# Kernel tuning notes

Measured on AMD Instinct MI355X. Metric: run time of the kernel, lower is better.

The kernel has to match this reference:

```python
import jax, jax.numpy as jnp
import numpy as np

LEAK = 0.01  # torch LeakyReLU default negative_slope

def lrelu(x):
    return jnp.where(x >= 0, x, LEAK * x)

def edge_conv(x, src, dst, ea, W1, b1, W2, b2):
    # message: cat(x_i=target, x_j=source, edge_attr) -> Linear -> LeakyReLU -> Linear
    m = jnp.concatenate([x[dst], x[src], ea], axis=1)          # [E, 2F+Fe]
    h = lrelu(m @ W1 + b1) @ W2 + b2                            # [E, H]
    n = x.shape[0]
    agg = jnp.full((n, h.shape[1]), jnp.inf, h.dtype).at[dst].min(h)  # scatter-min at target
    return jnp.where(jnp.isfinite(agg), agg, jnp.zeros_like(agg))     # empty nodes -> 0


def setup_inputs() -> dict:
    key = jax.random.key(0)
    ks = jax.random.split(key, 20)
    B, N, E = 4, 20000, 640000
    NF, AD, EF, H = 2, 1, 1, 8
    inp = {
        "node_features": jax.random.randint(ks[0], (B, N, NF), 0, 10, dtype=jnp.int32),
        "actions": jax.random.normal(ks[1], (B, N), dtype=jnp.float32),
        "edge_index": jax.random.randint(ks[2], (B, 2, E), 0, N, dtype=jnp.int64),
        "edge_features": jax.random.normal(ks[3], (B, E, EF), dtype=jnp.float32),
    }
    d0 = NF + AD  # 3
    def lin(k, fin, fout):
        s = 1.0 / np.sqrt(fin)
        k1, k2 = jax.random.split(k)
        return (jax.random.uniform(k1, (fin, fout), jnp.float32, -s, s),
                jax.random.uniform(k2, (fout,), jnp.float32, -s, s))
    inp["c1_W1"], inp["c1_b1"] = lin(ks[4], 2 * d0 + EF, H)
    inp["c1_W2"], inp["c1_b2"] = lin(ks[5], H, H)
    inp["c2_W1"], inp["c2_b1"] = lin(ks[6], 2 * H + 1, H)
    inp["c2_W2"], inp["c2_b2"] = lin(ks[7], H, H)
    inp["c3_W1"], inp["c3_b1"] = lin(ks[8], 2 * H + 1, H)
    inp["c3_W2"], inp["c3_b2"] = lin(ks[9], H, H)
    inp["lin_W"], inp["lin_b"] = lin(ks[10], d0 + H, 1)
    return inp


def reference(node_features, actions, edge_index, edge_features,
              c1_W1, c1_b1, c1_W2, c1_b2,
              c2_W1, c2_b1, c2_W2, c2_b2,
              c3_W1, c3_b1, c3_W2, c3_b2,
              lin_W, lin_b):
    # x = int(node_features) concat actions  -> float
    x0 = jnp.concatenate([node_features.astype(jnp.int32).astype(jnp.float32),
                          actions[..., None]], axis=-1)  # [B,N,3]

    def per_graph(x0g, eig, eag):
        src, dst = eig[0], eig[1]  # flow source_to_target: x_j=src, x_i=dst
        h = lrelu(edge_conv(x0g, src, dst, eag, c1_W1, c1_b1, c1_W2, c1_b2))
        h = lrelu(edge_conv(h, src, dst, eag, c2_W1, c2_b1, c2_W2, c2_b2))
        h = lrelu(edge_conv(h, src, dst, eag, c3_W1, c3_b1, c3_W2, c3_b2))
        xc = jnp.concatenate([x0g, h], axis=1)  # [N, 3+8]
        return jnp.sum(xc, axis=0)              # sum-pool over nodes

    pooled = jax.vmap(per_graph)(x0, edge_index, edge_features)  # [B, 11]
    return pooled @ lin_W + lin_b  # [B, 1]
```

## Files before the change

### kernel.cpp

```cpp
#include <hip/hip_runtime.h>
#include <hip/hip_cooperative_groups.h>

#define LEAK 0.01f
#define BS 128
#define PCHUNK 4096
#define PT 512
#define CT 512
#define MAXNB 256
#define CPGMAX 256
#define BARSTRIDE 64

__device__ __forceinline__ float lrelu(float v) {
    return v >= 0.f ? v : LEAK * v;
}

__device__ __forceinline__ unsigned int fmin_encode(float x) {
    unsigned int u = __float_as_uint(x);
    return (u & 0x80000000u) ? ~u : (u | 0x80000000u);
}
__device__ __forceinline__ float fmin_decode(unsigned int k) {
    unsigned int u = (k & 0x80000000u) ? (k ^ 0x80000000u) : ~k;
    return __uint_as_float(u);
}

__device__ __forceinline__ unsigned int bf16_rne(float f) {
    unsigned int u = __float_as_uint(f);
    return (u + 0x7FFFu + ((u >> 16) & 1u)) >> 16;
}

__device__ __forceinline__ void block_add(float c, float* dst) {
    __shared__ float wsum[8];
#pragma unroll
    for (int off = 32; off > 0; off >>= 1) c += __shfl_down(c, off, 64);
    int lane = threadIdx.x & 63;
    int wave = threadIdx.x >> 6;
    if (lane == 0) wsum[wave] = c;
    __syncthreads();
    if (threadIdx.x == 0) {
        float s = 0.f;
        int nw = blockDim.x >> 6;
        for (int w = 0; w < nw; ++w) s += wsum[w];
        atomicAdd(dst, s);
    }
}

__device__ __forceinline__ void graph_barrier(int* bar, int target) {
    __syncthreads();
    if (threadIdx.x == 0) {
        __threadfence();
        __hip_atomic_fetch_add(bar, 1, __ATOMIC_RELEASE, __HIP_MEMORY_SCOPE_AGENT);
        while (__hip_atomic_load(bar, __ATOMIC_RELAXED, __HIP_MEMORY_SCOPE_AGENT) <
               target)
            __builtin_amdgcn_s_sleep(2);
        __threadfence();
    }
    __syncthreads();
}


__device__ __forceinline__ void init_body(
    const int* __restrict__ nf, const float* __restrict__ act,
    const float* __restrict__ W1, const float* __restrict__ b1,
    const float* __restrict__ lw, const float* __restrict__ lb,
    float* __restrict__ a1, unsigned short* __restrict__ a2,
    float* __restrict__ out, int N, int b, int ib) {
    int t = threadIdx.x;
    int n = ib * PT + t;
    float c = 0.f;
    if (n < N) {
        size_t i = (size_t)b * N + n;
        float x0 = (float)nf[i * 2 + 0];
        float x1 = (float)nf[i * 2 + 1];
        float x2 = act[i];
        float v1[8], v2[8];
#pragma unroll
        for (int j = 0; j < 8; ++j) {
            v1[j] = b1[j] + x0 * W1[0 * 8 + j] + x1 * W1[1 * 8 + j] + x2 * W1[2 * 8 + j];
            v2[j] =         x0 * W1[3 * 8 + j] + x1 * W1[4 * 8 + j] + x2 * W1[5 * 8 + j];
        }
        float4* o1 = (float4*)(a1 + i * 8);
        o1[0] = make_float4(v1[0], v1[1], v1[2], v1[3]);
        o1[1] = make_float4(v1[4], v1[5], v1[6], v1[7]);
        unsigned int w[4];
#pragma unroll
        for (int q = 0; q < 4; ++q)
            w[q] = bf16_rne(v2[2 * q]) | (bf16_rne(v2[2 * q + 1]) << 16);
        *(int4*)(a2 + i * 8) = make_int4(w[0], w[1], w[2], w[3]);
        c = x0 * lw[0] + x1 * lw[1] + x2 * lw[2];
        if (n == 0) c += lb[0];
    }
    block_add(c, &out[b]);
}

__device__ __forceinline__ void part_body(
    const int* __restrict__ ei, const float* __restrict__ ea,
    int2* __restrict__ pairs, int* __restrict__ ofs,
    int E, int NB, int CPG, int b, int c,
    int* __restrict__ lc, int* __restrict__ lofs, int* __restrict__ ts) {
    int t = threadIdx.x;
    for (int i = t; i < NB; i += PT) lc[i] = 0;
    __syncthreads();

    int e0 = c * PCHUNK;
    int end = min(e0 + PCHUNK, E);
    const int* srow = ei + (size_t)b * 2 * E;
    const int* drow = srow + E;

    int pk[PCHUNK / PT];
#pragma unroll
    for (int j = 0; j < PCHUNK / PT; ++j) {
        int e = e0 + j * PT + t;
        int p = -1;
        if (e < end) {
            int d = drow[e];
            int bin = d >> 7;
            int r = atomicAdd(&lc[bin], 1);
            p = bin | ((d & 127) << 10) | (r << 17);
        }
        pk[j] = p;
    }
    __syncthreads();

    int v = (t < NB) ? lc[t] : 0;
    ts[t] = v;
    __syncthreads();
    int incl = v;
    for (int off = 1; off < PT; off <<= 1) {
        int add = (t >= off) ? ts[t - off] : 0;
        __syncthreads();
        incl += add;
        ts[t] = incl;
        __syncthreads();
    }
    if (t < NB) lofs[t] = incl - v;
    if (t == PT - 1) lofs[NB] = incl;
    __syncthreads();

    for (int i = t; i <= NB; i += PT) {
        int w = lofs[i];
        ofs[((size_t)b * (NB + 1) + i) * CPG + c] = w;
        if (i < NB) lc[i] = w;
    }
    __syncthreads();

    size_t pbase = (size_t)b * E + e0;
#pragma unroll
    for (int j = 0; j < PCHUNK / PT; ++j) {
        int e = e0 + j * PT + t;
        if (e < end) {
            int p = pk[j];
            int bin = p & 1023;
            int dl = (p >> 10) & 127;
            int r = p >> 17;
            int pos = lc[bin] + r;
            pairs[pbase + pos] =
                make_int2(srow[e] | (dl << 16), __float_as_int(ea[(size_t)b * E + e]));
        }
    }
}

__device__ __forceinline__ void conv_edge_compute(
    const float* we, const float* bb, const float* __restrict__ W2,
    int2 p, int4 raw, const float* __restrict__ a1s,
    unsigned int* __restrict__ acc) {
    int dl = (p.x >> 16) & 127;
    float eav = __int_as_float(p.y);
    unsigned int wq[4] = {(unsigned int)raw.x, (unsigned int)raw.y,
                          (unsigned int)raw.z, (unsigned int)raw.w};
    float a2v[8];
#pragma unroll
    for (int q = 0; q < 4; ++q) {
        a2v[2 * q]     = __uint_as_float(wq[q] << 16);
        a2v[2 * q + 1] = __uint_as_float(wq[q] & 0xFFFF0000u);
    }
    float h1[8];
#pragma unroll
    for (int j = 0; j < 8; ++j) {
        h1[j] = a1s[dl * 9 + j] + a2v[j];
        h1[j] = fmaf(eav, we[j], h1[j]);
        h1[j] = lrelu(h1[j]);
    }
    float h2[8];
#pragma unroll
    for (int j = 0; j < 8; ++j) h2[j] = bb[j];
#pragma unroll
    for (int kk = 0; kk < 8; ++kk) {
        float hk = h1[kk];
#pragma unroll
        for (int j = 0; j < 8; ++j) h2[j] = fmaf(hk, W2[kk * 8 + j], h2[j]);
    }
#pragma unroll
    for (int j = 0; j < 8; ++j)
        atomicMin(&acc[dl * 9 + j], fmin_encode(h2[j]));
}

__device__ __forceinline__ void conv_edges_runs(
    const unsigned short* __restrict__ a2g, const float* we, const float* bb,
    const float* __restrict__ W2, const int2* __restrict__ pairsg,
    const int* __restrict__ ofb, int CPG,
    const float* __restrict__ a1s, unsigned int* __restrict__ acc,
    int* __restrict__ rs, int* __restrict__ re) {
    int t = threadIdx.x;
    for (int c = t; c < CPG; c += CT) {
        rs[c] = ofb[c];
        re[c] = ofb[CPG + c];
    }
    __syncthreads();
    int sw = t >> 5, sub = t & 31;
    const int nsw = CT >> 5;
    for (int c = sw; c < CPG; c += nsw) {
        int cb = c * PCHUNK;
        int k1 = cb + re[c];
        for (int k = cb + rs[c] + sub; k < k1; k += 32) {
            int2 p = pairsg[k];
            int4 v = *(const int4*)(a2g + (size_t)(p.x & 0xFFFF) * 8);
            conv_edge_compute(we, bb, W2, p, v, a1s, acc);
        }
    }
}

__device__ __forceinline__ void conv_mid_body(
    const float* __restrict__ a1, const unsigned short* __restrict__ a2,
    const float* __restrict__ w1e, const float* __restrict__ W2,
    const float* __restrict__ b2,
    const float* __restrict__ nW1, const float* __restrict__ nb1,
    const int* __restrict__ ofs, const int2* __restrict__ pairs,
    float* __restrict__ na1, unsigned short* __restrict__ na2,
    int N, int NB, int CPG, int E, int b, int bin,
    float* __restrict__ a1s, unsigned int* __restrict__ acc,
    int* __restrict__ rs, int* __restrict__ re) {
    int n0 = bin << 7;
    int nCnt = min(BS, N - n0);
    int t = threadIdx.x;
    size_t node0 = (size_t)b * N + n0;

    for (int i = t; i < nCnt * 8; i += CT)
        a1s[(i >> 3) * 9 + (i & 7)] = a1[node0 * 8 + i];
    for (int i = t; i < BS * 9; i += CT) acc[i] = 0xFFFFFFFFu;
    float we[8], bb[8];
#pragma unroll
    for (int j = 0; j < 8; ++j) { we[j] = w1e[j]; bb[j] = b2[j]; }
    __syncthreads();

    conv_edges_runs(a2 + (size_t)b * N * 8, we, bb, W2,
                    pairs + (size_t)b * E,
                    ofs + ((size_t)b * (NB + 1) + bin) * CPG,
                    CPG, a1s, acc, rs, re);
    __syncthreads();

    for (int i = t; i < nCnt * 8; i += CT) {
        float v = fmin_decode(acc[(i >> 3) * 9 + (i & 7)]);
        unsigned int u = __float_as_uint(v);
        if ((u & 0x7F800000u) == 0x7F800000u) v = 0.f;
        a1s[(i >> 3) * 9 + (i & 7)] = lrelu(v);
    }
    __syncthreads();

    for (int nh = t; nh < nCnt * 2; nh += CT) {
        int node = nh >> 1, half = nh & 1;
        float h[8];
#pragma unroll
        for (int j = 0; j < 8; ++j) h[j] = a1s[node * 9 + j];
        float v[8];
#pragma unroll
        for (int j = 0; j < 8; ++j) v[j] = half ? 0.f : nb1[j];
        const float* Wbase = nW1 + (half ? 64 : 0);
#pragma unroll
        for (int k = 0; k < 8; ++k) {
            float hk = h[k];
#pragma unroll
            for (int j = 0; j < 8; ++j) v[j] = fmaf(hk, Wbase[k * 8 + j], v[j]);
        }
        if (half) {
            unsigned int w[4];
#pragma unroll
            for (int q = 0; q < 4; ++q)
                w[q] = bf16_rne(v[2 * q]) | (bf16_rne(v[2 * q + 1]) << 16);
            *(int4*)(na2 + (node0 + node) * 8) = make_int4(w[0], w[1], w[2], w[3]);
        } else {
            float4* o = (float4*)(na1 + (node0 + node) * 8);
            o[0] = make_float4(v[0], v[1], v[2], v[3]);
            o[1] = make_float4(v[4], v[5], v[6], v[7]);
        }
    }
    __syncthreads();
}

__device__ __forceinline__ void conv_final_body(
    const float* __restrict__ a1, const unsigned short* __restrict__ a2,
    const float* __restrict__ w1e, const float* __restrict__ W2,
    const float* __restrict__ b2, const float* __restrict__ lw,
    const int* __restrict__ ofs, const int2* __restrict__ pairs,
    float* __restrict__ out, int N, int NB, int CPG, int E, int b, int bin,
    float* __restrict__ a1s, unsigned int* __restrict__ acc,
    int* __restrict__ rs, int* __restrict__ re) {
    int n0 = bin << 7;
    int nCnt = min(BS, N - n0);
    int t = threadIdx.x;
    size_t node0 = (size_t)b * N + n0;

    for (int i = t; i < nCnt * 8; i += CT)
        a1s[(i >> 3) * 9 + (i & 7)] = a1[node0 * 8 + i];
    for (int i = t; i < BS * 9; i += CT) acc[i] = 0xFFFFFFFFu;
    float we[8], bb[8];
#pragma unroll
    for (int j = 0; j < 8; ++j) { we[j] = w1e[j]; bb[j] = b2[j]; }
    __syncthreads();

    conv_edges_runs(a2 + (size_t)b * N * 8, we, bb, W2,
                    pairs + (size_t)b * E,
                    ofs + ((size_t)b * (NB + 1) + bin) * CPG,
                    CPG, a1s, acc, rs, re);
    __syncthreads();

    float c = 0.f;
    if (t < nCnt) {
#pragma unroll
        for (int j = 0; j < 8; ++j) {
            float v = fmin_decode(acc[t * 9 + j]);
            unsigned int u = __float_as_uint(v);
            if ((u & 0x7F800000u) == 0x7F800000u) v = 0.f;
            c = fmaf(lrelu(v), lw[3 + j], c);
        }
    }
    __syncthreads();
    block_add(c, &out[b]);
}


struct MegaParams {
    const int* ei; const float* ea;
    int2* pairs; int* ofs;
    const int* nf; const float* act;
    const float* W11; const float* b11; const float* W21; const float* b21;
    const float* W12; const float* b12; const float* W22; const float* b22;
    const float* W13; const float* b13; const float* W23; const float* b23;
    const float* lw; const float* lb;
    float* a1A; unsigned short* a2A; float* a1B; unsigned short* a2B;
    float* out;
    int* bar;
    int E, N, NB, CPG, initBlocks;
};

__global__ __launch_bounds__(512, 8) void mega_kernel(MegaParams P) {
    __shared__ int lc[MAXNB];
    __shared__ int lofs[MAXNB + 1];
    __shared__ int ts[PT];
    __shared__ float a1s[BS * 9];
    __shared__ unsigned int acc[BS * 9];
    __shared__ int rs[CPGMAX];
    __shared__ int re[CPGMAX];
    int b = blockIdx.y, bx = blockIdx.x;
    int* bar = P.bar + b * BARSTRIDE;
    const int gx = gridDim.x;

    if (bx < P.CPG)
        part_body(P.ei, P.ea, P.pairs, P.ofs, P.E, P.NB, P.CPG, b, bx, lc, lofs, ts);
    else if (bx - P.CPG < P.initBlocks)
        init_body(P.nf, P.act, P.W11, P.b11, P.lw, P.lb, P.a1A, P.a2A, P.out,
                  P.N, b, bx - P.CPG);
    graph_barrier(bar, gx);
    if (bx < P.NB)
        conv_mid_body(P.a1A, P.a2A, P.W11 + 6 * 8, P.W21, P.b21, P.W12, P.b12,
                      P.ofs, P.pairs, P.a1B, P.a2B, P.N, P.NB, P.CPG, P.E,
                      b, bx, a1s, acc, rs, re);
    graph_barrier(bar, gx * 2);
    if (bx < P.NB)
        conv_mid_body(P.a1B, P.a2B, P.W12 + 16 * 8, P.W22, P.b22, P.W13, P.b13,
                      P.ofs, P.pairs, P.a1A, P.a2A, P.N, P.NB, P.CPG, P.E,
                      b, bx, a1s, acc, rs, re);
    graph_barrier(bar, gx * 3);
    if (bx < P.NB)
        conv_final_body(P.a1A, P.a2A, P.W13 + 16 * 8, P.W23, P.b23, P.lw,
                        P.ofs, P.pairs, P.out, P.N, P.NB, P.CPG, P.E,
                        b, bx, a1s, acc, rs, re);
}


__global__ __launch_bounds__(PT) void part_init_kernel(
    const int* __restrict__ ei, const float* __restrict__ ea,
    int2* __restrict__ pairs, int* __restrict__ ofs,
    const int* __restrict__ nf, const float* __restrict__ act,
    const float* __restrict__ W1, const float* __restrict__ b1,
    const float* __restrict__ lw, const float* __restrict__ lb,
    float* __restrict__ a1, unsigned short* __restrict__ a2,
    float* __restrict__ out, int E, int N, int NB, int CPG) {
    __shared__ int lc[MAXNB];
    __shared__ int lofs[MAXNB + 1];
    __shared__ int ts[PT];
    int b = blockIdx.y;
    if (blockIdx.x >= CPG) {
        init_body(nf, act, W1, b1, lw, lb, a1, a2, out, N, b, blockIdx.x - CPG);
        return;
    }
    part_body(ei, ea, pairs, ofs, E, NB, CPG, b, blockIdx.x, lc, lofs, ts);
}

__global__ __launch_bounds__(CT) void conv_mid_kernel(
    const float* __restrict__ a1, const unsigned short* __restrict__ a2,
    const float* __restrict__ w1e, const float* __restrict__ W2,
    const float* __restrict__ b2,
    const float* __restrict__ nW1, const float* __restrict__ nb1,
    const int* __restrict__ ofs, const int2* __restrict__ pairs,
    float* __restrict__ na1, unsigned short* __restrict__ na2,
    int N, int NB, int CPG, int E) {
    __shared__ float a1s[BS * 9];
    __shared__ unsigned int acc[BS * 9];
    __shared__ int rs[CPGMAX];
    __shared__ int re[CPGMAX];
    conv_mid_body(a1, a2, w1e, W2, b2, nW1, nb1, ofs, pairs, na1, na2,
                  N, NB, CPG, E, blockIdx.y, blockIdx.x, a1s, acc, rs, re);
}

__global__ __launch_bounds__(CT) void conv_final_kernel(
    const float* __restrict__ a1, const unsigned short* __restrict__ a2,
    const float* __restrict__ w1e, const float* __restrict__ W2,
    const float* __restrict__ b2, const float* __restrict__ lw,
    const int* __restrict__ ofs, const int2* __restrict__ pairs,
    float* __restrict__ out, int N, int NB, int CPG, int E) {
    __shared__ float a1s[BS * 9];
    __shared__ unsigned int acc[BS * 9];
    __shared__ int rs[CPGMAX];
    __shared__ int re[CPGMAX];
    conv_final_body(a1, a2, w1e, W2, b2, lw, ofs, pairs, out,
                    N, NB, CPG, E, blockIdx.y, blockIdx.x, a1s, acc, rs, re);
}


__global__ __launch_bounds__(256) void node_init_kernel(
    const int* __restrict__ nf, const float* __restrict__ act,
    float* __restrict__ x0, int BN) {
    int tid = blockIdx.x * blockDim.x + threadIdx.x;
    if (tid >= BN) return;
    x0[tid * 3 + 0] = (float)nf[tid * 2 + 0];
    x0[tid * 3 + 1] = (float)nf[tid * 2 + 1];
    x0[tid * 3 + 2] = act[tid];
}

template <int D>
__global__ __launch_bounds__(256) void edge_conv_kernel(
    const float* __restrict__ x, const int* __restrict__ ei,
    const float* __restrict__ ea,
    const float* __restrict__ W1, const float* __restrict__ b1,
    const float* __restrict__ W2, const float* __restrict__ b2,
    unsigned int* __restrict__ agg, int E, int N, int B) {
    int tid = blockIdx.x * blockDim.x + threadIdx.x;
    if (tid >= B * E) return;
    int b = tid / E;
    int e = tid - b * E;
    const int* eb = ei + (size_t)b * 2 * E;
    int s = eb[e];
    int d = eb[E + e];
    const float* xi = x + ((size_t)b * N + d) * D;
    const float* xj = x + ((size_t)b * N + s) * D;
    constexpr int M = 2 * D + 1;
    float m[M];
#pragma unroll
    for (int k = 0; k < D; ++k) { m[k] = xi[k]; m[D + k] = xj[k]; }
    m[2 * D] = ea[(size_t)b * E + e];
    float h1[8];
#pragma unroll
    for (int j = 0; j < 8; ++j) h1[j] = b1[j];
#pragma unroll
    for (int k = 0; k < M; ++k) {
        float mk = m[k];
#pragma unroll
        for (int j = 0; j < 8; ++j) h1[j] = fmaf(mk, W1[k * 8 + j], h1[j]);
    }
#pragma unroll
    for (int j = 0; j < 8; ++j) h1[j] = lrelu(h1[j]);
    float h2[8];
#pragma unroll
    for (int j = 0; j < 8; ++j) h2[j] = b2[j];
#pragma unroll
    for (int k = 0; k < 8; ++k) {
        float hk = h1[k];
#pragma unroll
        for (int j = 0; j < 8; ++j) h2[j] = fmaf(hk, W2[k * 8 + j], h2[j]);
    }
    unsigned int* ag = agg + ((size_t)b * N + d) * 8;
#pragma unroll
    for (int j = 0; j < 8; ++j) atomicMin(&ag[j], fmin_encode(h2[j]));
}

__global__ __launch_bounds__(256) void finalize_kernel(
    unsigned int* __restrict__ agg, int total) {
    int tid = blockIdx.x * blockDim.x + threadIdx.x;
    if (tid >= total) return;
    float v = fmin_decode(agg[tid]);
    unsigned int u = __float_as_uint(v);
    if ((u & 0x7F800000u) == 0x7F800000u) v = 0.f;
    ((float*)agg)[tid] = lrelu(v);
}

__global__ __launch_bounds__(256) void pool_kernel(
    const float* __restrict__ x0, const float* __restrict__ h,
    const float* __restrict__ lw, const float* __restrict__ lb,
    float* __restrict__ out, int N) {
    int b = blockIdx.y;
    int n = blockIdx.x * blockDim.x + threadIdx.x;
    float c = 0.f;
    if (n < N) {
        const float* x = x0 + ((size_t)b * N + n) * 3;
        const float* hh = h + ((size_t)b * N + n) * 8;
        c = x[0] * lw[0] + x[1] * lw[1] + x[2] * lw[2];
#pragma unroll
        for (int k = 0; k < 8; ++k) c = fmaf(hh[k], lw[3 + k], c);
        if (n == 0) c += lb[0];
    }
    block_add(c, &out[b]);
}


static inline size_t align256(size_t x) { return (x + 255) & ~(size_t)255; }

extern "C" void kernel_launch(void* const* d_in, const int* in_sizes, int n_in,
                              void* d_out, int out_size, void* d_ws, size_t ws_size,
                              hipStream_t stream) {
    const int B = 4;
    const int N = in_sizes[1] / B;
    const int E = in_sizes[2] / (2 * B);

    const int*   nf  = (const int*)d_in[0];
    const float* act = (const float*)d_in[1];
    const int*   ei  = (const int*)d_in[2];
    const float* ea  = (const float*)d_in[3];
    const float* c1_W1 = (const float*)d_in[4];
    const float* c1_b1 = (const float*)d_in[5];
    const float* c1_W2 = (const float*)d_in[6];
    const float* c1_b2 = (const float*)d_in[7];
    const float* c2_W1 = (const float*)d_in[8];
    const float* c2_b1 = (const float*)d_in[9];
    const float* c2_W2 = (const float*)d_in[10];
    const float* c2_b2 = (const float*)d_in[11];
    const float* c3_W1 = (const float*)d_in[12];
    const float* c3_b1 = (const float*)d_in[13];
    const float* c3_W2 = (const float*)d_in[14];
    const float* c3_b2 = (const float*)d_in[15];
    const float* lw    = (const float*)d_in[16];
    const float* lb    = (const float*)d_in[17];
    float* out = (float*)d_out;

    const int BN = B * N;
    const int BE = B * E;
    const int NB = (N + BS - 1) / BS;
    const int CPG = (E + PCHUNK - 1) / PCHUNK;
    const int initBlocks = (N + PT - 1) / PT;

    char* ws = (char*)d_ws;
    size_t off = 0;
    float* a1A = (float*)(ws + off);           off += align256((size_t)BN * 8 * 4);
    float* a1B = (float*)(ws + off);           off += align256((size_t)BN * 8 * 4);
    unsigned short* a2A = (unsigned short*)(ws + off); off += align256((size_t)BN * 8 * 2);
    unsigned short* a2B = (unsigned short*)(ws + off); off += align256((size_t)BN * 8 * 2);
    int* ofs    = (int*)(ws + off);    off += align256((size_t)B * (NB + 1) * CPG * 4);
    int2* pairs = (int2*)(ws + off);   off += align256((size_t)BE * 8);
    float* x0   = (float*)(ws + off);  off += align256((size_t)BN * 3 * 4);
    int* bar    = (int*)(ws + off);    off += align256((size_t)B * BARSTRIDE * 4);
    const bool useFast = (off <= ws_size) && (NB <= MAXNB) && (CPG <= CPGMAX) &&
                         (N <= 32768);

    hipMemsetAsync(out, 0, (size_t)B * sizeof(float), stream);

    if (useFast) {
        const int gx = (CPG + initBlocks > NB) ? (CPG + initBlocks) : NB;

        int dev = 0;
        hipGetDevice(&dev);
        int numCU = 0;
        hipDeviceGetAttribute(&numCU, hipDeviceAttributeMultiprocessorCount, dev);
        int occ = 0;
        hipOccupancyMaxActiveBlocksPerMultiprocessor(&occ, mega_kernel, 512, 0);
        const bool canCoop = (occ > 0) && ((size_t)occ * (size_t)numCU >=
                                           (size_t)gx * (size_t)B);

        if (canCoop) {
            hipMemsetAsync(bar, 0, (size_t)B * BARSTRIDE * sizeof(int), stream);
            MegaParams P;
            P.ei = ei; P.ea = ea; P.pairs = pairs; P.ofs = ofs;
            P.nf = nf; P.act = act;
            P.W11 = c1_W1; P.b11 = c1_b1; P.W21 = c1_W2; P.b21 = c1_b2;
            P.W12 = c2_W1; P.b12 = c2_b1; P.W22 = c2_W2; P.b22 = c2_b2;
            P.W13 = c3_W1; P.b13 = c3_b1; P.W23 = c3_W2; P.b23 = c3_b2;
            P.lw = lw; P.lb = lb;
            P.a1A = a1A; P.a2A = a2A; P.a1B = a1B; P.a2B = a2B;
            P.out = out; P.bar = bar;
            P.E = E; P.N = N; P.NB = NB; P.CPG = CPG; P.initBlocks = initBlocks;
            void* args[] = {&P};
            hipLaunchCooperativeKernel((void*)mega_kernel, dim3(gx, B),
                                       dim3(512), args, 0, stream);
        } else {
            dim3 pgrid(CPG + initBlocks, B);
            dim3 cgrid(NB, B);
            part_init_kernel<<<pgrid, PT, 0, stream>>>(
                ei, ea, pairs, ofs, nf, act, c1_W1, c1_b1, lw, lb,
                a1A, a2A, out, E, N, NB, CPG);
            conv_mid_kernel<<<cgrid, CT, 0, stream>>>(
                a1A, a2A, c1_W1 + 6 * 8, c1_W2, c1_b2, c2_W1, c2_b1,
                ofs, pairs, a1B, a2B, N, NB, CPG, E);
            conv_mid_kernel<<<cgrid, CT, 0, stream>>>(
                a1B, a2B, c2_W1 + 16 * 8, c2_W2, c2_b2, c3_W1, c3_b1,
                ofs, pairs, a1A, a2A, N, NB, CPG, E);
            conv_final_kernel<<<cgrid, CT, 0, stream>>>(
                a1A, a2A, c3_W1 + 16 * 8, c3_W2, c3_b2, lw,
                ofs, pairs, out, N, NB, CPG, E);
        }
    } else {
        const int egrid = (BE + 255) / 256;
        const int aggTotal = BN * 8;
        const int agrid = (aggTotal + 255) / 256;
        const size_t aggBytes = (size_t)aggTotal * 4;
        unsigned int* uA = (unsigned int*)a1A;
        unsigned int* uB = (unsigned int*)a1B;

        node_init_kernel<<<(BN + 255) / 256, 256, 0, stream>>>(nf, act, x0, BN);

        hipMemsetAsync(uA, 0xFF, aggBytes, stream);
        edge_conv_kernel<3><<<egrid, 256, 0, stream>>>(
            x0, ei, ea, c1_W1, c1_b1, c1_W2, c1_b2, uA, E, N, B);
        finalize_kernel<<<agrid, 256, 0, stream>>>(uA, aggTotal);

        hipMemsetAsync(uB, 0xFF, aggBytes, stream);
        edge_conv_kernel<8><<<egrid, 256, 0, stream>>>(
            (const float*)uA, ei, ea, c2_W1, c2_b1, c2_W2, c2_b2, uB, E, N, B);
        finalize_kernel<<<agrid, 256, 0, stream>>>(uB, aggTotal);

        hipMemsetAsync(uA, 0xFF, aggBytes, stream);
        edge_conv_kernel<8><<<egrid, 256, 0, stream>>>(
            (const float*)uB, ei, ea, c3_W1, c3_b1, c3_W2, c3_b2, uA, E, N, B);
        finalize_kernel<<<agrid, 256, 0, stream>>>(uA, aggTotal);

        dim3 plgrid((N + 255) / 256, B);
        pool_kernel<<<plgrid, 256, 0, stream>>>(x0, (const float*)uA, lw, lb, out, N);
    }
}
```

Baseline: 208.6 us.

## Compact partitioned edge pairs into contiguous per-bin ranges before conv layers

Adds a compaction phase that gathers each destination bin's edge runs, which are scattered across many partition chunks, into one contiguous array with global per-bin offsets computed by prefix scans. The three conv layers then stream a dense range with all threads instead of walking many short per-chunk runs with 32-lane subwarps, aiming to cut load imbalance and idle lanes. The cost is an extra grid barrier and pass that copies every edge pair once, plus a second pairs buffer in the workspace.

```diff
diff --git a/kernel.cpp b/kernel.cpp
--- a/kernel.cpp
+++ b/kernel.cpp
@@ -159,6 +159,59 @@
     }
 }
 
+__device__ __forceinline__ void compact_body(
+    const int* __restrict__ ofs, const int2* __restrict__ pairs,
+    int2* __restrict__ cpairs, int* __restrict__ gofs,
+    int E, int NB, int CPG, int b, int bin,
+    int* __restrict__ rs, int* __restrict__ re, int* __restrict__ cs,
+    int* __restrict__ redsum) {
+    int t = threadIdx.x;
+    const int* ofb = ofs + ((size_t)b * (NB + 1) + bin) * CPG;
+    if (t == 0) *redsum = 0;
+    for (int i = t; i < CPGMAX; i += CT) cs[i] = 0;
+    __syncthreads();
+
+    int lsum = 0;
+    for (int c = t; c < CPG; c += CT) {
+        int s = ofb[c];
+        int len = ofb[CPG + c] - s;
+        rs[c] = s;
+        re[c] = len;
+        cs[c] = len;
+        lsum += s;
+    }
+#pragma unroll
+    for (int off = 32; off > 0; off >>= 1) lsum += __shfl_down(lsum, off, 64);
+    if ((t & 63) == 0 && lsum != 0) atomicAdd(redsum, lsum);
+    __syncthreads();
+
+    for (int off = 1; off < CPGMAX; off <<= 1) {
+        int a = 0;
+        if (t < CPGMAX) { a = cs[t]; if (t >= off) a += cs[t - off]; }
+        __syncthreads();
+        if (t < CPGMAX) cs[t] = a;
+        __syncthreads();
+    }
+    int base = *redsum;
+    int* gofsb = gofs + (size_t)b * (NB + 1);
+    if (t == 0) {
+        gofsb[bin] = base;
+        if (bin == NB - 1) gofsb[NB] = base + cs[CPG - 1];
+    }
+
+    const int2* pg = pairs + (size_t)b * E;
+    int2* cp = cpairs + (size_t)b * E;
+    int w = t >> 6, lane = t & 63;
+    const int nw = CT >> 6;
+    for (int c = w; c < CPG; c += nw) {
+        int len = re[c];
+        int src = c * PCHUNK + rs[c];
+        int dst = base + cs[c] - len;
+        for (int i = lane; i < len; i += 64)
+            cp[dst + i] = pg[src + i];
+    }
+}
+
 __device__ __forceinline__ void conv_edge_compute(
     const float* we, const float* bb, const float* __restrict__ W2,
     int2 p, int4 raw, const float* __restrict__ a1s,
@@ -194,28 +247,15 @@
         atomicMin(&acc[dl * 9 + j], fmin_encode(h2[j]));
 }
 
-__device__ __forceinline__ void conv_edges_runs(
+__device__ __forceinline__ void conv_edges_dense(
     const unsigned short* __restrict__ a2g, const float* we, const float* bb,
-    const float* __restrict__ W2, const int2* __restrict__ pairsg,
-    const int* __restrict__ ofb, int CPG,
-    const float* __restrict__ a1s, unsigned int* __restrict__ acc,
-    int* __restrict__ rs, int* __restrict__ re) {
-    int t = threadIdx.x;
-    for (int c = t; c < CPG; c += CT) {
-        rs[c] = ofb[c];
-        re[c] = ofb[CPG + c];
-    }
-    __syncthreads();
-    int sw = t >> 5, sub = t & 31;
-    const int nsw = CT >> 5;
-    for (int c = sw; c < CPG; c += nsw) {
-        int cb = c * PCHUNK;
-        int k1 = cb + re[c];
-        for (int k = cb + rs[c] + sub; k < k1; k += 32) {
-            int2 p = pairsg[k];
-            int4 v = *(const int4*)(a2g + (size_t)(p.x & 0xFFFF) * 8);
-            conv_edge_compute(we, bb, W2, p, v, a1s, acc);
-        }
+    const float* __restrict__ W2, const int2* __restrict__ cpg,
+    int start, int end,
+    const float* __restrict__ a1s, unsigned int* __restrict__ acc) {
+    for (int k = start + (int)threadIdx.x; k < end; k += CT) {
+        int2 p = cpg[k];
+        int4 v = *(const int4*)(a2g + (size_t)(p.x & 0xFFFF) * 8);
+        conv_edge_compute(we, bb, W2, p, v, a1s, acc);
     }
 }
 
@@ -224,11 +264,10 @@
     const float* __restrict__ w1e, const float* __restrict__ W2,
     const float* __restrict__ b2,
     const float* __restrict__ nW1, const float* __restrict__ nb1,
-    const int* __restrict__ ofs, const int2* __restrict__ pairs,
+    const int* __restrict__ gofs, const int2* __restrict__ cpairs,
     float* __restrict__ na1, unsigned short* __restrict__ na2,
-    int N, int NB, int CPG, int E, int b, int bin,
-    float* __restrict__ a1s, unsigned int* __restrict__ acc,
-    int* __restrict__ rs, int* __restrict__ re) {
+    int N, int NB, int E, int b, int bin,
+    float* __restrict__ a1s, unsigned int* __restrict__ acc) {
     int n0 = bin << 7;
     int nCnt = min(BS, N - n0);
     int t = threadIdx.x;
@@ -240,12 +279,13 @@
     float we[8], bb[8];
 #pragma unroll
     for (int j = 0; j < 8; ++j) { we[j] = w1e[j]; bb[j] = b2[j]; }
-    __syncthreads();
-
-    conv_edges_runs(a2 + (size_t)b * N * 8, we, bb, W2,
-                    pairs + (size_t)b * E,
-                    ofs + ((size_t)b * (NB + 1) + bin) * CPG,
-                    CPG, a1s, acc, rs, re);
+    const int* gofsb = gofs + (size_t)b * (NB + 1);
+    int start = gofsb[bin];
+    int end = gofsb[bin + 1];
+    __syncthreads();
+
+    conv_edges_dense(a2 + (size_t)b * N * 8, we, bb, W2,
+                     cpairs + (size_t)b * E, start, end, a1s, acc);
     __syncthreads();
 
     for (int i = t; i < nCnt * 8; i += CT) {
@@ -290,10 +330,9 @@
     const float* __restrict__ a1, const unsigned short* __restrict__ a2,
     const float* __restrict__ w1e, const float* __restrict__ W2,
     const float* __restrict__ b2, const float* __restrict__ lw,
-    const int* __restrict__ ofs, const int2* __restrict__ pairs,
-    float* __restrict__ out, int N, int NB, int CPG, int E, int b, int bin,
-    float* __restrict__ a1s, unsigned int* __restrict__ acc,
-    int* __restrict__ rs, int* __restrict__ re) {
+    const int* __restrict__ gofs, const int2* __restrict__ cpairs,
+    float* __restrict__ out, int N, int NB, int E, int b, int bin,
+    float* __restrict__ a1s, unsigned int* __restrict__ acc) {
     int n0 = bin << 7;
     int nCnt = min(BS, N - n0);
     int t = threadIdx.x;
@@ -305,12 +344,13 @@
     float we[8], bb[8];
 #pragma unroll
     for (int j = 0; j < 8; ++j) { we[j] = w1e[j]; bb[j] = b2[j]; }
-    __syncthreads();
-
-    conv_edges_runs(a2 + (size_t)b * N * 8, we, bb, W2,
-                    pairs + (size_t)b * E,
-                    ofs + ((size_t)b * (NB + 1) + bin) * CPG,
-                    CPG, a1s, acc, rs, re);
+    const int* gofsb = gofs + (size_t)b * (NB + 1);
+    int start = gofsb[bin];
+    int end = gofsb[bin + 1];
+    __syncthreads();
+
+    conv_edges_dense(a2 + (size_t)b * N * 8, we, bb, W2,
+                     cpairs + (size_t)b * E, start, end, a1s, acc);
     __syncthreads();
 
     float c = 0.f;
@@ -331,6 +371,7 @@
 struct MegaParams {
     const int* ei; const float* ea;
     int2* pairs; int* ofs;
+    int2* cpairs; int* gofs;
     const int* nf; const float* act;
     const float* W11; const float* b11; const float* W21; const float* b21;
     const float* W12; const float* b12; const float* W22; const float* b22;
@@ -350,6 +391,8 @@
     __shared__ unsigned int acc[BS * 9];
     __shared__ int rs[CPGMAX];
     __shared__ int re[CPGMAX];
+    __shared__ int cs[CPGMAX];
+    __shared__ int redsum;
     int b = blockIdx.y, bx = blockIdx.x;
     int* bar = P.bar + b * BARSTRIDE;
     const int gx = gridDim.x;
@@ -361,19 +404,23 @@
                   P.N, b, bx - P.CPG);
     graph_barrier(bar, gx);
     if (bx < P.NB)
-        conv_mid_body(P.a1A, P.a2A, P.W11 + 6 * 8, P.W21, P.b21, P.W12, P.b12,
-                      P.ofs, P.pairs, P.a1B, P.a2B, P.N, P.NB, P.CPG, P.E,
-                      b, bx, a1s, acc, rs, re);
+        compact_body(P.ofs, P.pairs, P.cpairs, P.gofs, P.E, P.NB, P.CPG,
+                     b, bx, rs, re, cs, &redsum);
     graph_barrier(bar, gx * 2);
     if (bx < P.NB)
-        conv_mid_body(P.a1B, P.a2B, P.W12 + 16 * 8, P.W22, P.b22, P.W13, P.b13,
-                      P.ofs, P.pairs, P.a1A, P.a2A, P.N, P.NB, P.CPG, P.E,
-                      b, bx, a1s, acc, rs, re);
+        conv_mid_body(P.a1A, P.a2A, P.W11 + 6 * 8, P.W21, P.b21, P.W12, P.b12,
+                      P.gofs, P.cpairs, P.a1B, P.a2B, P.N, P.NB, P.E,
+                      b, bx, a1s, acc);
     graph_barrier(bar, gx * 3);
     if (bx < P.NB)
+        conv_mid_body(P.a1B, P.a2B, P.W12 + 16 * 8, P.W22, P.b22, P.W13, P.b13,
+                      P.gofs, P.cpairs, P.a1A, P.a2A, P.N, P.NB, P.E,
+                      b, bx, a1s, acc);
+    graph_barrier(bar, gx * 4);
+    if (bx < P.NB)
         conv_final_body(P.a1A, P.a2A, P.W13 + 16 * 8, P.W23, P.b23, P.lw,
-                        P.ofs, P.pairs, P.out, P.N, P.NB, P.CPG, P.E,
-                        b, bx, a1s, acc, rs, re);
+                        P.gofs, P.cpairs, P.out, P.N, P.NB, P.E,
+                        b, bx, a1s, acc);
 }
 
 
@@ -396,34 +443,42 @@
     part_body(ei, ea, pairs, ofs, E, NB, CPG, b, blockIdx.x, lc, lofs, ts);
 }
 
+__global__ __launch_bounds__(CT) void compact_kernel(
+    const int* __restrict__ ofs, const int2* __restrict__ pairs,
+    int2* __restrict__ cpairs, int* __restrict__ gofs,
+    int E, int NB, int CPG) {
+    __shared__ int rs[CPGMAX];
+    __shared__ int re[CPGMAX];
+    __shared__ int cs[CPGMAX];
+    __shared__ int redsum;
+    compact_body(ofs, pairs, cpairs, gofs, E, NB, CPG,
+                 blockIdx.y, blockIdx.x, rs, re, cs, &redsum);
+}
+
 __global__ __launch_bounds__(CT) void conv_mid_kernel(
     const float* __restrict__ a1, const unsigned short* __restrict__ a2,
     const float* __restrict__ w1e, const float* __restrict__ W2,
     const float* __restrict__ b2,
     const float* __restrict__ nW1, const float* __restrict__ nb1,
-    const int* __restrict__ ofs, const int2* __restrict__ pairs,
+    const int* __restrict__ gofs, const int2* __restrict__ cpairs,
     float* __restrict__ na1, unsigned short* __restrict__ na2,
-    int N, int NB, int CPG, int E) {
+    int N, int NB, int E) {
     __shared__ float a1s[BS * 9];
     __shared__ unsigned int acc[BS * 9];
-    __shared__ int rs[CPGMAX];
-    __shared__ int re[CPGMAX];
-    conv_mid_body(a1, a2, w1e, W2, b2, nW1, nb1, ofs, pairs, na1, na2,
-                  N, NB, CPG, E, blockIdx.y, blockIdx.x, a1s, acc, rs, re);
+    conv_mid_body(a1, a2, w1e, W2, b2, nW1, nb1, gofs, cpairs, na1, na2,
+                  N, NB, E, blockIdx.y, blockIdx.x, a1s, acc);
 }
 
 __global__ __launch_bounds__(CT) void conv_final_kernel(
     const float* __restrict__ a1, const unsigned short* __restrict__ a2,
     const float* __restrict__ w1e, const float* __restrict__ W2,
     const float* __restrict__ b2, const float* __restrict__ lw,
-    const int* __restrict__ ofs, const int2* __restrict__ pairs,
-    float* __restrict__ out, int N, int NB, int CPG, int E) {
+    const int* __restrict__ gofs, const int2* __restrict__ cpairs,
+    float* __restrict__ out, int N, int NB, int E) {
     __shared__ float a1s[BS * 9];
     __shared__ unsigned int acc[BS * 9];
-    __shared__ int rs[CPGMAX];
-    __shared__ int re[CPGMAX];
-    conv_final_body(a1, a2, w1e, W2, b2, lw, ofs, pairs, out,
-                    N, NB, CPG, E, blockIdx.y, blockIdx.x, a1s, acc, rs, re);
+    conv_final_body(a1, a2, w1e, W2, b2, lw, gofs, cpairs, out,
+                    N, NB, E, blockIdx.y, blockIdx.x, a1s, acc);
 }
 
 
@@ -555,6 +610,8 @@
     unsigned short* a2B = (unsigned short*)(ws + off); off += align256((size_t)BN * 8 * 2);
     int* ofs    = (int*)(ws + off);    off += align256((size_t)B * (NB + 1) * CPG * 4);
     int2* pairs = (int2*)(ws + off);   off += align256((size_t)BE * 8);
+    int2* cpairs = (int2*)(ws + off);  off += align256((size_t)BE * 8);
+    int* gofs   = (int*)(ws + off);    off += align256((size_t)B * (NB + 1) * 4);
     float* x0   = (float*)(ws + off);  off += align256((size_t)BN * 3 * 4);
     int* bar    = (int*)(ws + off);    off += align256((size_t)B * BARSTRIDE * 4);
     const bool useFast = (off <= ws_size) && (NB <= MAXNB) && (CPG <= CPGMAX) &&
@@ -578,6 +635,7 @@
             hipMemsetAsync(bar, 0, (size_t)B * BARSTRIDE * sizeof(int), stream);
             MegaParams P;
             P.ei = ei; P.ea = ea; P.pairs = pairs; P.ofs = ofs;
+            P.cpairs = cpairs; P.gofs = gofs;
             P.nf = nf; P.act = act;
             P.W11 = c1_W1; P.b11 = c1_b1; P.W21 = c1_W2; P.b21 = c1_b2;
             P.W12 = c2_W1; P.b12 = c2_b1; P.W22 = c2_W2; P.b22 = c2_b2;
@@ -595,15 +653,17 @@
             part_init_kernel<<<pgrid, PT, 0, stream>>>(
                 ei, ea, pairs, ofs, nf, act, c1_W1, c1_b1, lw, lb,
                 a1A, a2A, out, E, N, NB, CPG);
+            compact_kernel<<<cgrid, CT, 0, stream>>>(
+                ofs, pairs, cpairs, gofs, E, NB, CPG);
             conv_mid_kernel<<<cgrid, CT, 0, stream>>>(
                 a1A, a2A, c1_W1 + 6 * 8, c1_W2, c1_b2, c2_W1, c2_b1,
-                ofs, pairs, a1B, a2B, N, NB, CPG, E);
+                gofs, cpairs, a1B, a2B, N, NB, E);
             conv_mid_kernel<<<cgrid, CT, 0, stream>>>(
                 a1B, a2B, c2_W1 + 16 * 8, c2_W2, c2_b2, c3_W1, c3_b1,
-                ofs, pairs, a1A, a2A, N, NB, CPG, E);
+                gofs, cpairs, a1A, a2A, N, NB, E);
             conv_final_kernel<<<cgrid, CT, 0, stream>>>(
                 a1A, a2A, c3_W1 + 16 * 8, c3_W2, c3_b2, lw,
-                ofs, pairs, out, N, NB, CPG, E);
+                gofs, cpairs, out, N, NB, E);
         }
     } else {
         const int egrid = (BE + 255) / 256;
```

Result: faster. 199.1 us (-4.6%).
